# Kernel tuning notes

Measured on AMD Instinct MI355X. Metric: run time of the kernel, lower is better.

Reference implementation:

```python
import jax, jax.numpy as jnp
import numpy as np

B, LAT, ADIM, NACT, H = 131072, 64, 16, 9, 128

def setup_inputs() -> dict:
    key = jax.random.key(0)
    ks = jax.random.split(key, 24)
    p = lambda k, shp: (jax.random.normal(k, shp, dtype=jnp.float32) * 0.05)
    return {
        "z_t": jax.random.normal(ks[0], (B, LAT), dtype=jnp.float32),
        "action": jax.random.randint(ks[1], (B,), 0, NACT),
        "hidden": jnp.zeros((1, B, H), dtype=jnp.float32),
        "embed": p(ks[2], (NACT, ADIM)),
        "fuse_W": p(ks[3], (H, LAT + ADIM)), "fuse_b": p(ks[4], (H,)),
        "W_ih": p(ks[5], (3 * H, H)), "W_hh": p(ks[6], (3 * H, H)),
        "b_ih": p(ks[7], (3 * H,)), "b_hh": p(ks[8], (3 * H,)),
        "ns_W1": p(ks[9], (H, H)), "ns_b1": p(ks[10], (H,)),
        "ns_W2": p(ks[11], (LAT, H)), "ns_b2": p(ks[12], (LAT,)),
        "rw_W1": p(ks[13], (H // 2, H)), "rw_b1": p(ks[14], (H // 2,)),
        "rw_W2": p(ks[15], (1, H // 2)), "rw_b2": p(ks[16], (1,)),
        "dn_W1": p(ks[17], (H // 2, H)), "dn_b1": p(ks[18], (H // 2,)),
        "dn_W2": p(ks[19], (1, H // 2)), "dn_b2": p(ks[20], (1,)),
    }

def _mlp2(x, W1, b1, W2, b2):
    return jax.nn.relu(x @ W1.T + b1) @ W2.T + b2

def reference(z_t, action, hidden, embed, fuse_W, fuse_b, W_ih, W_hh, b_ih, b_hh,
              ns_W1, ns_b1, ns_W2, ns_b2, rw_W1, rw_b1, rw_W2, rw_b2,
              dn_W1, dn_b1, dn_W2, dn_b2):
    a_emb = embed[action]                                  # [B, ADIM]
    fused = jnp.concatenate([z_t, a_emb], axis=-1)         # [B, LAT+ADIM]
    x = jax.nn.relu(fused @ fuse_W.T + fuse_b)             # [B, H]
    h0 = hidden[0]                                         # [B, H]
    gi = x @ W_ih.T + b_ih                                 # [B, 3H]
    gh = h0 @ W_hh.T + b_hh                                # [B, 3H]
    Hd = x.shape[-1]
    r = jax.nn.sigmoid(gi[:, :Hd] + gh[:, :Hd])
    zg = jax.nn.sigmoid(gi[:, Hd:2 * Hd] + gh[:, Hd:2 * Hd])
    n = jnp.tanh(gi[:, 2 * Hd:] + r * gh[:, 2 * Hd:])
    h_new = (1.0 - zg) * n + zg * h0                       # [B, H]
    out = h_new
    z_next = _mlp2(out, ns_W1, ns_b1, ns_W2, ns_b2)        # [B, LAT]
    reward = _mlp2(out, rw_W1, rw_b1, rw_W2, rw_b2)        # [B, 1]
    done_logit = _mlp2(out, dn_W1, dn_b1, dn_W2, dn_b2)    # [B, 1]
    return (z_next, reward, done_logit, h_new[None])
```

## Files before the change

### kernel.cpp

```cpp
#include <hip/hip_runtime.h>
#include <hip/hip_bf16.h>
#include <cstddef>
#include <cstdint>

#define BATCH 131072
#define HOFF ((size_t)BATCH * 66)

typedef __attribute__((ext_vector_type(8))) short short8;
typedef __attribute__((ext_vector_type(4))) short short4v;
typedef __attribute__((ext_vector_type(4))) float f32x4;
typedef __attribute__((ext_vector_type(16))) float f32x16;

typedef const __attribute__((address_space(1))) unsigned int* gas_t;
typedef __attribute__((address_space(3))) unsigned int* las_t;

#define WS_GRU    13312
#define WS_GUNIT  26112
#define WS_HEAD   117760
#define WS_ELEMS  161280

#define G_BASE    13312
#define STR_BASE  65536

#define MFMA32(a,b,c) __builtin_amdgcn_mfma_f32_32x32x16_bf16((a),(b),(c),0,0,0)

__device__ __forceinline__ short f2bf(float x) {
    __hip_bfloat16 b = __float2bfloat16(x);
    return __builtin_bit_cast(short, b);
}
__device__ __forceinline__ float bf2f(short s) {
    unsigned u = ((unsigned)(unsigned short)s) << 16;
    return __builtin_bit_cast(float, u);
}
__device__ __forceinline__ float fsigmoid(float x) { return __builtin_amdgcn_rcpf(1.0f + __expf(-x)); }
__device__ __forceinline__ float ftanh(float x)    { return 1.0f - 2.0f * __builtin_amdgcn_rcpf(1.0f + __expf(2.0f * x)); }

__device__ __forceinline__ short8 packbf(f32x4 a, f32x4 b) {
    short8 r;
    r[0]=f2bf(a[0]); r[1]=f2bf(a[1]); r[2]=f2bf(a[2]); r[3]=f2bf(a[3]);
    r[4]=f2bf(b[0]); r[5]=f2bf(b[1]); r[6]=f2bf(b[2]); r[7]=f2bf(b[3]);
    return r;
}

template<int NCH>
__device__ __forceinline__ void stage_lds(const short* __restrict__ src, short* dst, int t) {
    constexpr int NP = (NCH + 511) / 512;
    #pragma unroll
    for (int k = 0; k < NP; ++k) {
        int c = t + 512 * k;
        if ((NCH % 512 == 0) || c < NCH)
            __builtin_amdgcn_global_load_lds((gas_t)(const void*)(src + (size_t)c * 8),
                                             (las_t)(void*)(dst + (size_t)c * 8), 16, 0, 0);
    }
}

extern "C" __global__ void prep_weights(const float* __restrict__ fuse_W,
                                        const float* __restrict__ W_ih, const float* __restrict__ W_hh,
                                        const float* __restrict__ ns_W1, const float* __restrict__ ns_W2,
                                        const float* __restrict__ rw_W1, const float* __restrict__ dn_W1,
                                        short* __restrict__ ws) {
    int i = blockIdx.x * 256 + threadIdx.x;
    if (i >= WS_ELEMS) return;
    float v = 0.f;
    if (i < WS_GRU) {
        int j = i / 104, k = i % 104;
        if (k < 80) v = fuse_W[j*80 + k];
    } else if (i < WS_HEAD) {
        int rel = i - WS_GRU;
        int u2 = rel / WS_GUNIT, e = rel % WS_GUNIT;
        int rb = e / 136, k = e % 136;
        if (k < 128) {
            int gp = rb >> 5, r = rb & 31;
            int g = gp >> 1, p = gp & 1;
            const float* W = p ? W_hh : W_ih;
            v = W[(size_t)(g*128 + u2*32 + r)*128 + k];
        }
    } else {
        int rel = i - WS_HEAD;
        int h = rel / 4352, e = rel % 4352;
        int r = e / 136, k = e % 136;
        if (k < 128) {
            const float* W; int rb;
            if (h < 4)      { W = ns_W1; rb = h*32; }
            else if (h < 6) { W = ns_W2; rb = (h-4)*32; }
            else if (h < 8) { W = rw_W1; rb = (h-6)*32; }
            else            { W = dn_W1; rb = (h-8)*32; }
            v = W[(size_t)(rb + r)*128 + k];
        }
    }
    ws[i] = f2bf(v);
}

#define GRU_J2(U, J2) do {                                                                 \
    const int ub = G_BASE + (U)*WS_GUNIT;                                                  \
    const int cb = (J2)*32 + ln;                                                           \
    const float br  = b_ih[cb]       + b_hh[cb];                                           \
    const float bz  = b_ih[128 + cb] + b_hh[128 + cb];                                     \
    const float bin = b_ih[256 + cb];                                                      \
    const float bhn = b_hh[256 + cb];                                                      \
    f32x16 ar = zz16, az = zz16, ain = zz16, ahn = zz16;                                   \
    _Pragma("unroll") for (int kf = 0; kf < 8; ++kf) {                                     \
        const int ko = kf*16 + hb8;                                                        \
        short8 B0 = *(const short8*)&smem[ub + (0*32 + ln)*136 + ko];                      \
        ar  = MFMA32(xa[kf], B0, ar);                                                      \
        short8 B1 = *(const short8*)&smem[ub + (1*32 + ln)*136 + ko];                      \
        ar  = MFMA32(ha[kf], B1, ar);                                                      \
        short8 B2 = *(const short8*)&smem[ub + (2*32 + ln)*136 + ko];                      \
        az  = MFMA32(xa[kf], B2, az);                                                      \
        short8 B3 = *(const short8*)&smem[ub + (3*32 + ln)*136 + ko];                      \
        az  = MFMA32(ha[kf], B3, az);                                                      \
        short8 B4 = *(const short8*)&smem[ub + (4*32 + ln)*136 + ko];                      \
        ain = MFMA32(xa[kf], B4, ain);                                                     \
        short8 B5 = *(const short8*)&smem[ub + (5*32 + ln)*136 + ko];                      \
        ahn = MFMA32(ha[kf], B5, ahn);                                                     \
    }                                                                                      \
    _Pragma("unroll") for (int p = 0; p < 8; ++p) {                                        \
        unsigned hp = h0d[J2][p];                                                          \
        _Pragma("unroll") for (int q = 0; q < 2; ++q) {                                    \
            const int reg = 2*p + q;                                                       \
            float h0v = bf2f((short)(q ? (hp >> 16) : (hp & 0xffffu)));                    \
            float rg = fsigmoid(ar[reg] + br);                                             \
            float zg = fsigmoid(az[reg] + bz);                                             \
            float ng = ftanh(ain[reg] + bin + rg*(ahn[reg] + bhn));                        \
            S[((reg&3) + 8*(reg>>2) + hr4)*40 + ln] = f2bf((1.f - zg)*ng + zg*h0v);        \
        }                                                                                  \
    }                                                                                      \
} while (0)

#define HEAD32(FRAG, BIASEXPR, HU, RELU) do {                                              \
    f32x16 a = zz16;                                                                       \
    _Pragma("unroll") for (int kf = 0; kf < 8; ++kf) {                                     \
        short8 B = *(const short8*)&smem[G_BASE + (HU)*4352 + ln*136 + kf*16 + hb8];       \
        a = MFMA32((FRAG)[kf], B, a);                                                      \
    }                                                                                      \
    const float bb = (BIASEXPR);                                                           \
    _Pragma("unroll") for (int reg = 0; reg < 16; ++reg) {                                 \
        float v = a[reg] + bb;                                                             \
        if (RELU) v = fmaxf(v, 0.f);                                                       \
        S[((reg&3) + 8*(reg>>2) + hr4)*40 + ln] = f2bf(v);                                 \
    }                                                                                      \
} while (0)

extern "C" __global__ __launch_bounds__(512, 1)
void gru_mfma(const float* __restrict__ z_t, const int* __restrict__ action,
              const float* __restrict__ hidden, const float* __restrict__ embed,
              const float* __restrict__ fuse_b,
              const float* __restrict__ b_ih, const float* __restrict__ b_hh,
              const float* __restrict__ ns_b1, const float* __restrict__ ns_b2,
              const float* __restrict__ rw_b1, const float* __restrict__ rw_W2, const float* __restrict__ rw_b2,
              const float* __restrict__ dn_b1, const float* __restrict__ dn_W2, const float* __restrict__ dn_b2,
              const short* __restrict__ ws, float* out)
{
    __shared__ __align__(16) short smem[75776];

    const int t    = threadIdx.x;
    const int lane = t & 63;
    const int w    = t >> 6;
    const int ln   = lane & 31;
    const int hb8  = (lane >> 5) * 8;
    const int hr4  = (lane >> 5) * 4;
    const int R    = blockIdx.x * 256 + w * 32;
    short* const S = &smem[STR_BASE + w * 1280];

    const f32x16 zz16 = {0,0,0,0,0,0,0,0,0,0,0,0,0,0,0,0};

    auto store_hnew = [&](int j2) {
        #pragma unroll
        for (int v = 0; v < 4; ++v) {
            int idx = v*64 + lane;
            int r = idx >> 3, c = (idx & 7) * 4;
            short4v s = *(const short4v*)&S[r*40 + c];
            f32x4 f = { bf2f(s[0]), bf2f(s[1]), bf2f(s[2]), bf2f(s[3]) };
            *(f32x4*)&out[HOFF + (size_t)(R + r)*128 + j2*32 + c] = f;
        }
    };
    auto store_z = [&](int q) {
        #pragma unroll
        for (int v = 0; v < 4; ++v) {
            int idx = v*64 + lane;
            int r = idx >> 3, c = (idx & 7) * 4;
            short4v s = *(const short4v*)&S[r*40 + c];
            f32x4 f = { bf2f(s[0]), bf2f(s[1]), bf2f(s[2]), bf2f(s[3]) };
            *(f32x4*)&out[(size_t)(R + r)*64 + q*32 + c] = f;
        }
    };
    auto hpartial = [&](const float* W2, float acc) -> float {
        int rr = lane & 31;
        #pragma unroll
        for (int kk = 0; kk < 32; kk += 8) {
            short8 s = *(const short8*)&S[rr*40 + kk];
            f32x4 w0 = *(const f32x4*)&W2[kk];
            f32x4 w1 = *(const f32x4*)&W2[kk+4];
            acc += bf2f(s[0])*w0[0] + bf2f(s[1])*w0[1] + bf2f(s[2])*w0[2] + bf2f(s[3])*w0[3]
                 + bf2f(s[4])*w1[0] + bf2f(s[5])*w1[1] + bf2f(s[6])*w1[2] + bf2f(s[7])*w1[3];
        }
        return acc;
    };

    stage_lds<1664>(ws, &smem[0], t);
    stage_lds<6528>(ws + WS_GRU, &smem[G_BASE], t);

    short8 fa[5];
    short8 ha[8];
    {
        const int row = R + ln;
        #pragma unroll
        for (int kf = 0; kf < 4; ++kf) {
            f32x4 p0 = *(const f32x4*)&z_t[(size_t)row*64 + kf*16 + hb8];
            f32x4 p1 = *(const f32x4*)&z_t[(size_t)row*64 + kf*16 + hb8 + 4];
            fa[kf] = packbf(p0, p1);
        }
        int a = action[row];
        f32x4 e0 = *(const f32x4*)&embed[a*16 + hb8];
        f32x4 e1 = *(const f32x4*)&embed[a*16 + hb8 + 4];
        fa[4] = packbf(e0, e1);
        #pragma unroll
        for (int kf = 0; kf < 8; ++kf) {
            f32x4 p0 = *(const f32x4*)&hidden[(size_t)row*128 + kf*16 + hb8];
            f32x4 p1 = *(const f32x4*)&hidden[(size_t)row*128 + kf*16 + hb8 + 4];
            ha[kf] = packbf(p0, p1);
        }
    }

    unsigned h0d[4][8];
    #pragma unroll
    for (int n = 0; n < 4; ++n) {
        *(short8*)&S[ln*40 + hb8]      = ha[2*n];
        *(short8*)&S[ln*40 + 16 + hb8] = ha[2*n+1];
        #pragma unroll
        for (int p = 0; p < 8; ++p) {
            const int r0 = 2*p, r1 = 2*p + 1;
            unsigned a = (unsigned short)S[((r0&3) + 8*(r0>>2) + hr4)*40 + ln];
            unsigned b = (unsigned short)S[((r1&3) + 8*(r1>>2) + hr4)*40 + ln];
            h0d[n][p] = a | (b << 16);
        }
    }
    __syncthreads();

    short8 xa[8];
    #pragma unroll
    for (int n = 0; n < 4; ++n) {
        f32x16 a = zz16;
        #pragma unroll
        for (int kf = 0; kf < 5; ++kf) {
            short8 B = *(const short8*)&smem[(n*32 + ln)*104 + kf*16 + hb8];
            a = MFMA32(fa[kf], B, a);
        }
        float fb = fuse_b[n*32 + ln];
        #pragma unroll
        for (int reg = 0; reg < 16; ++reg)
            S[((reg&3) + 8*(reg>>2) + hr4)*40 + ln] = f2bf(fmaxf(a[reg] + fb, 0.f));
        xa[2*n]   = *(const short8*)&S[ln*40 + hb8];
        xa[2*n+1] = *(const short8*)&S[ln*40 + 16 + hb8];
    }

    short8 hfa[8];
    GRU_J2(0, 0);
    hfa[0] = *(const short8*)&S[ln*40 + hb8];
    hfa[1] = *(const short8*)&S[ln*40 + 16 + hb8];
    store_hnew(0);
    GRU_J2(1, 1);
    hfa[2] = *(const short8*)&S[ln*40 + hb8];
    hfa[3] = *(const short8*)&S[ln*40 + 16 + hb8];
    store_hnew(1);

    __syncthreads();
    stage_lds<6528>(ws + WS_GRU + 2*WS_GUNIT, &smem[G_BASE], t);
    __syncthreads();

    GRU_J2(0, 2);
    hfa[4] = *(const short8*)&S[ln*40 + hb8];
    hfa[5] = *(const short8*)&S[ln*40 + 16 + hb8];
    store_hnew(2);
    GRU_J2(1, 3);
    hfa[6] = *(const short8*)&S[ln*40 + hb8];
    hfa[7] = *(const short8*)&S[ln*40 + 16 + hb8];
    store_hnew(3);

    __syncthreads();
    stage_lds<5440>(ws + WS_HEAD, &smem[G_BASE], t);
    __syncthreads();

    short8 ta[8];
    HEAD32(hfa, ns_b1[ln],      0, true);
    ta[0] = *(const short8*)&S[ln*40 + hb8];
    ta[1] = *(const short8*)&S[ln*40 + 16 + hb8];
    HEAD32(hfa, ns_b1[32 + ln], 1, true);
    ta[2] = *(const short8*)&S[ln*40 + hb8];
    ta[3] = *(const short8*)&S[ln*40 + 16 + hb8];
    HEAD32(hfa, ns_b1[64 + ln], 2, true);
    ta[4] = *(const short8*)&S[ln*40 + hb8];
    ta[5] = *(const short8*)&S[ln*40 + 16 + hb8];
    HEAD32(hfa, ns_b1[96 + ln], 3, true);
    ta[6] = *(const short8*)&S[ln*40 + hb8];
    ta[7] = *(const short8*)&S[ln*40 + 16 + hb8];

    HEAD32(ta, ns_b2[ln],      4, false); store_z(0);
    HEAD32(ta, ns_b2[32 + ln], 5, false); store_z(1);

    float racc = rw_b2[0];
    HEAD32(hfa, rw_b1[ln],      6, true); racc = hpartial(rw_W2, racc);
    HEAD32(hfa, rw_b1[32 + ln], 7, true); racc = hpartial(rw_W2 + 32, racc);
    if (lane < 32) out[(size_t)BATCH*64 + R + ln] = racc;

    float dacc = dn_b2[0];
    HEAD32(hfa, dn_b1[ln],      8, true); dacc = hpartial(dn_W2, dacc);
    HEAD32(hfa, dn_b1[32 + ln], 9, true); dacc = hpartial(dn_W2 + 32, dacc);
    if (lane < 32) out[(size_t)BATCH*65 + R + ln] = dacc;
}

extern "C" void kernel_launch(void* const* d_in, const int* in_sizes, int n_in,
                              void* d_out, int out_size, void* d_ws, size_t ws_size,
                              hipStream_t stream) {
    const float* z_t    = (const float*)d_in[0];
    const int*   action = (const int*)  d_in[1];
    const float* hidden = (const float*)d_in[2];
    const float* embed  = (const float*)d_in[3];
    const float* fuse_W = (const float*)d_in[4];
    const float* fuse_b = (const float*)d_in[5];
    const float* W_ih   = (const float*)d_in[6];
    const float* W_hh   = (const float*)d_in[7];
    const float* b_ih   = (const float*)d_in[8];
    const float* b_hh   = (const float*)d_in[9];
    const float* ns_W1  = (const float*)d_in[10];
    const float* ns_b1  = (const float*)d_in[11];
    const float* ns_W2  = (const float*)d_in[12];
    const float* ns_b2  = (const float*)d_in[13];
    const float* rw_W1  = (const float*)d_in[14];
    const float* rw_b1  = (const float*)d_in[15];
    const float* rw_W2  = (const float*)d_in[16];
    const float* rw_b2  = (const float*)d_in[17];
    const float* dn_W1  = (const float*)d_in[18];
    const float* dn_b1  = (const float*)d_in[19];
    const float* dn_W2  = (const float*)d_in[20];
    const float* dn_b2  = (const float*)d_in[21];
    float* out = (float*)d_out;
    short* ws  = (short*)d_ws;

    hipLaunchKernelGGL(prep_weights, dim3((WS_ELEMS + 255) / 256), dim3(256), 0, stream,
                       fuse_W, W_ih, W_hh, ns_W1, ns_W2, rw_W1, dn_W1, ws);

    hipLaunchKernelGGL(gru_mfma, dim3(BATCH / 256), dim3(512), 0, stream,
                       z_t, action, hidden, embed,
                       fuse_b, b_ih, b_hh, ns_b1, ns_b2,
                       rw_b1, rw_W2, rw_b2, dn_b1, dn_W2, dn_b2,
                       ws, out);
}
```

Baseline: 92.29 us.

## Serialize GRU gate accumulators and compute h0 transpose on demand to cut registers

```diff
diff --git a/kernel.cpp b/kernel.cpp
--- a/kernel.cpp
+++ b/kernel.cpp
@@ -94,35 +94,64 @@
 #define GRU_J2(U, J2) do {                                                                 \
     const int ub = G_BASE + (U)*WS_GUNIT;                                                  \
     const int cb = (J2)*32 + ln;                                                           \
+                                 \
+    *(short8*)&S[ln*40 + hb8]      = ha[2*(J2)];                                           \
+    *(short8*)&S[ln*40 + 16 + hb8] = ha[2*(J2)+1];                                         \
+    unsigned h0p[8];                                                                       \
+    _Pragma("unroll") for (int p = 0; p < 8; ++p) {                                        \
+        const int r0 = 2*p, r1 = 2*p + 1;                                                  \
+        unsigned a = (unsigned short)S[((r0&3) + 8*(r0>>2) + hr4)*40 + ln];                \
+        unsigned b = (unsigned short)S[((r1&3) + 8*(r1>>2) + hr4)*40 + ln];                \
+        h0p[p] = a | (b << 16);                                                            \
+    }                                                                                      \
     const float br  = b_ih[cb]       + b_hh[cb];                                           \
     const float bz  = b_ih[128 + cb] + b_hh[128 + cb];                                     \
     const float bin = b_ih[256 + cb];                                                      \
     const float bhn = b_hh[256 + cb];                                                      \
-    f32x16 ar = zz16, az = zz16, ain = zz16, ahn = zz16;                                   \
+    f32x16 acc, tmp;                                                                       \
+                                                                  \
+    acc = zz16;                                                                            \
     _Pragma("unroll") for (int kf = 0; kf < 8; ++kf) {                                     \
         const int ko = kf*16 + hb8;                                                        \
         short8 B0 = *(const short8*)&smem[ub + (0*32 + ln)*136 + ko];                      \
-        ar  = MFMA32(xa[kf], B0, ar);                                                      \
+        acc = MFMA32(xa[kf], B0, acc);                                                     \
         short8 B1 = *(const short8*)&smem[ub + (1*32 + ln)*136 + ko];                      \
-        ar  = MFMA32(ha[kf], B1, ar);                                                      \
+        acc = MFMA32(ha[kf], B1, acc);                                                     \
+    }                                                                                      \
+    _Pragma("unroll") for (int reg = 0; reg < 16; ++reg)                                   \
+        tmp[reg] = fsigmoid(acc[reg] + br);                                                \
+                                                                \
+    acc = zz16;                                                                            \
+    _Pragma("unroll") for (int kf = 0; kf < 8; ++kf) {                                     \
+        short8 B5 = *(const short8*)&smem[ub + (5*32 + ln)*136 + kf*16 + hb8];             \
+        acc = MFMA32(ha[kf], B5, acc);                                                     \
+    }                                                                                      \
+    _Pragma("unroll") for (int reg = 0; reg < 16; ++reg)                                   \
+        tmp[reg] = tmp[reg] * (acc[reg] + bhn);                                            \
+                                                            \
+    acc = zz16;                                                                            \
+    _Pragma("unroll") for (int kf = 0; kf < 8; ++kf) {                                     \
+        short8 B4 = *(const short8*)&smem[ub + (4*32 + ln)*136 + kf*16 + hb8];             \
+        acc = MFMA32(xa[kf], B4, acc);                                                     \
+    }                                                                                      \
+    _Pragma("unroll") for (int reg = 0; reg < 16; ++reg)                                   \
+        tmp[reg] = ftanh(acc[reg] + bin + tmp[reg]);                                       \
+                                             \
+    acc = zz16;                                                                            \
+    _Pragma("unroll") for (int kf = 0; kf < 8; ++kf) {                                     \
+        const int ko = kf*16 + hb8;                                                        \
         short8 B2 = *(const short8*)&smem[ub + (2*32 + ln)*136 + ko];                      \
-        az  = MFMA32(xa[kf], B2, az);                                                      \
+        acc = MFMA32(xa[kf], B2, acc);                                                     \
         short8 B3 = *(const short8*)&smem[ub + (3*32 + ln)*136 + ko];                      \
-        az  = MFMA32(ha[kf], B3, az);                                                      \
-        short8 B4 = *(const short8*)&smem[ub + (4*32 + ln)*136 + ko];                      \
-        ain = MFMA32(xa[kf], B4, ain);                                                     \
-        short8 B5 = *(const short8*)&smem[ub + (5*32 + ln)*136 + ko];                      \
-        ahn = MFMA32(ha[kf], B5, ahn);                                                     \
+        acc = MFMA32(ha[kf], B3, acc);                                                     \
     }                                                                                      \
     _Pragma("unroll") for (int p = 0; p < 8; ++p) {                                        \
-        unsigned hp = h0d[J2][p];                                                          \
+        unsigned hp = h0p[p];                                                              \
         _Pragma("unroll") for (int q = 0; q < 2; ++q) {                                    \
             const int reg = 2*p + q;                                                       \
             float h0v = bf2f((short)(q ? (hp >> 16) : (hp & 0xffffu)));                    \
-            float rg = fsigmoid(ar[reg] + br);                                             \
-            float zg = fsigmoid(az[reg] + bz);                                             \
-            float ng = ftanh(ain[reg] + bin + rg*(ahn[reg] + bhn));                        \
-            S[((reg&3) + 8*(reg>>2) + hr4)*40 + ln] = f2bf((1.f - zg)*ng + zg*h0v);        \
+            float zg = fsigmoid(acc[reg] + bz);                                            \
+            S[((reg&3) + 8*(reg>>2) + hr4)*40 + ln] = f2bf((1.f - zg)*tmp[reg] + zg*h0v);  \
         }                                                                                  \
     }                                                                                      \
 } while (0)
@@ -219,20 +248,6 @@
             f32x4 p0 = *(const f32x4*)&hidden[(size_t)row*128 + kf*16 + hb8];
             f32x4 p1 = *(const f32x4*)&hidden[(size_t)row*128 + kf*16 + hb8 + 4];
             ha[kf] = packbf(p0, p1);
-        }
-    }
-
-    unsigned h0d[4][8];
-    #pragma unroll
-    for (int n = 0; n < 4; ++n) {
-        *(short8*)&S[ln*40 + hb8]      = ha[2*n];
-        *(short8*)&S[ln*40 + 16 + hb8] = ha[2*n+1];
-        #pragma unroll
-        for (int p = 0; p < 8; ++p) {
-            const int r0 = 2*p, r1 = 2*p + 1;
-            unsigned a = (unsigned short)S[((r0&3) + 8*(r0>>2) + hr4)*40 + ln];
-            unsigned b = (unsigned short)S[((r1&3) + 8*(r1>>2) + hr4)*40 + ln];
-            h0d[n][p] = a | (b << 16);
         }
     }
     __syncthreads();
```

After: 78.34 us. -15.1%, faster.
